# Performance work log

Hardware: AMD Instinct MI355X
Metric: run time of the kernel (lower is better)

Reference implementation:

```python
import jax, jax.numpy as jnp
import numpy as np

K = 8                      # batch_k
NONZERO_CUTOFF = 1.4       # nonzero_loss_cutoff
MARGIN = 1.0               # F.triplet_margin_loss default (module's margin arg is unused)
PD_EPS = 1e-6              # torch pairwise_distance eps


def setup_inputs() -> dict:
    key = jax.random.key(0)
    x = jax.random.normal(key, (4096, 128), dtype=jnp.float32)
    return {"x": x}


def _sample_indices(x, key):
    """Distance-weighted negative sampling; returns (a_idx, p_idx, n_idx), each [n*(K-1)]."""
    n, d = x.shape
    # per-row L2 normalize (eps added to norm, as in original)
    xn = x / (jnp.sqrt(jnp.sum(x * x, axis=1, keepdims=True)) + 1e-5)
    # pairwise euclidean distance; identity added under sqrt exactly as original
    sq = jnp.sum(xn * xn, axis=1, keepdims=True)               # [n,1]
    dist2 = sq + sq.T - 2.0 * (xn @ xn.T)                       # [n,n]
    dist = jnp.sqrt(dist2 + jnp.eye(n, dtype=x.dtype))          # [n,n]
    # distance-weighted sampling log-weights (Wu et al.)
    log_w = (2.0 - d) * jnp.log(dist) - (d - 3) / 2.0 * jnp.log(1.0 - 0.25 * dist * dist)
    w = jnp.exp(log_w - jnp.max(log_w))
    # block mask: same-block pairs excluded
    block = jnp.arange(n) // K                                  # [n]
    mask = (block[:, None] != block[None, :]).astype(x.dtype)
    w = w * mask * (dist < NONZERO_CUTOFF).astype(x.dtype)
    row_sum = jnp.sum(w, axis=1, keepdims=True)
    # rows where weights are degenerate fall back to uniform (original's try/except)
    valid = jnp.isfinite(row_sum) & (row_sum > 0) & jnp.all(jnp.isfinite(w), axis=1, keepdims=True)
    logits = jnp.where(valid, jnp.where(w > 0, jnp.log(w), -jnp.inf), 0.0)   # [n,n]
    # batched categorical sampling via Gumbel-max: K-1 negatives per anchor
    g = jax.random.gumbel(key, (n, K - 1, n), dtype=jnp.float32)
    n_idx = jnp.argmax(logits[:, None, :] + g, axis=-1).reshape(-1)          # [n*(K-1)]
    # anchor/positive pairs: for each i, all other members of its block
    r = jnp.arange(n) % K                                       # position in block
    off = jnp.arange(K - 1)
    p_off = jnp.where(off[None, :] < r[:, None], off[None, :], off[None, :] + 1)
    p_idx = (block[:, None] * K + p_off).reshape(-1)            # [n*(K-1)]
    a_idx = jnp.repeat(jnp.arange(n), K - 1)                    # [n*(K-1)]
    return a_idx, p_idx, n_idx


def reference(x) -> jnp.ndarray:
    key = jax.random.key(42)
    a_idx, p_idx, n_idx = _sample_indices(x, key)
    a, p, ng = x[a_idx], x[p_idx], x[n_idx]
    d_ap = jnp.sqrt(jnp.sum((a - p + PD_EPS) ** 2, axis=1))
    d_an = jnp.sqrt(jnp.sum((a - ng + PD_EPS) ** 2, axis=1))
    return jnp.mean(jnp.maximum(d_ap - d_an + MARGIN, 0.0))
```

## Files before the change

kernel.cpp:

```cpp
#include <hip/hip_runtime.h>
#include <stdint.h>

#define NROWS 4096
#define DIM   128
#define KB    8
#define NS    7
#define TCH   16
#define HALF_CNT 58720256u

typedef __bf16 v8bf __attribute__((ext_vector_type(8)));
typedef float  v4f  __attribute__((ext_vector_type(4)));

__device__ __forceinline__ uint32_t rotl32(uint32_t x, int r) {
    return (x << r) | (x >> (32 - r));
}

__device__ __forceinline__ void threefry2x32(uint32_t c0, uint32_t c1,
                                             uint32_t& o0, uint32_t& o1) {
    const uint32_t ks0 = 0u;
    const uint32_t ks1 = 42u;
    const uint32_t ks2 = 0x1BD11BDAu ^ ks0 ^ ks1;
    uint32_t x0 = c0 + ks0;
    uint32_t x1 = c1 + ks1;
#define TF_R(r) { x0 += x1; x1 = rotl32(x1, r); x1 ^= x0; }
    TF_R(13) TF_R(15) TF_R(26) TF_R(6)
    x0 += ks1; x1 += ks2 + 1u;
    TF_R(17) TF_R(29) TF_R(16) TF_R(24)
    x0 += ks2; x1 += ks0 + 2u;
    TF_R(13) TF_R(15) TF_R(26) TF_R(6)
    x0 += ks0; x1 += ks1 + 3u;
    TF_R(17) TF_R(29) TF_R(16) TF_R(24)
    x0 += ks1; x1 += ks2 + 4u;
    TF_R(13) TF_R(15) TF_R(26) TF_R(6)
    x0 += ks2; x1 += ks0 + 5u;
#undef TF_R
    o0 = x0; o1 = x1;
}

__device__ __forceinline__ float gumbel_of(uint32_t b) {
    float f = __uint_as_float((b >> 9) | 0x3f800000u) - 1.0f;
    float u = f + 1.17549435e-38f;
    float l1 = __log2f(u);
    float inner = -0.69314718055994531f * l1;
    float l2 = __log2f(inner);
    return -0.69314718055994531f * l2;
}

__global__ void knorm(const float* __restrict__ x, __bf16* __restrict__ xh,
                      __bf16* __restrict__ xl, float* __restrict__ sqv) {
    const int i = blockIdx.x;
    const int t = threadIdx.x;
    float2 v = ((const float2*)(x + (size_t)i * DIM))[t];
    float s = v.x * v.x + v.y * v.y;
#pragma unroll
    for (int m = 32; m > 0; m >>= 1) s += __shfl_xor(s, m, 64);
    float norm = sqrtf(s) + 1e-5f;
    float ox = v.x / norm, oy = v.y / norm;
    __bf16 hx = (__bf16)ox, hy = (__bf16)oy;
    float lx = ox - (float)hx, ly = oy - (float)hy;
    union { __bf16 b[2]; uint32_t u; } ph, pl;
    ph.b[0] = hx; ph.b[1] = hy;
    pl.b[0] = (__bf16)lx; pl.b[1] = (__bf16)ly;
    ((uint32_t*)xh)[i * 64 + t] = ph.u;
    ((uint32_t*)xl)[i * 64 + t] = pl.u;
    float s2 = ox * ox + oy * oy;
#pragma unroll
    for (int m = 32; m > 0; m >>= 1) s2 += __shfl_xor(s2, m, 64);
    if (t == 0) sqv[i] = s2;
}

__global__ __launch_bounds__(256, 2) void ksample(
        const __bf16* __restrict__ xh, const __bf16* __restrict__ xl,
        const float* __restrict__ sqv,
        float* __restrict__ pV, int* __restrict__ pI) {
    const int lane  = threadIdx.x & 63;
    const int chunk = (blockIdx.x << 2) + (threadIdx.x >> 6);
    const int grp   = blockIdx.y;
    const int rlo = lane & 15;
    const int khi = lane >> 4;

    const int afr = grp * 8 + (rlo >> 1) + ((rlo & 1) << 11);
    v8bf ah[4], al[4];
#pragma unroll
    for (int ks = 0; ks < 4; ++ks) {
        const size_t off = (size_t)afr * DIM + ks * 32 + khi * 8;
        ah[ks] = *(const v8bf*)(xh + off);
        al[ks] = *(const v8bf*)(xl + off);
    }

    const int base = grp * 8 + khi * 2;
    float sqA[4];
    sqA[0] = sqv[base];
    sqA[1] = sqv[base + 2048];
    sqA[2] = sqv[base + 1];
    sqA[3] = sqv[base + 2049];
    const uint32_t P0 = (uint32_t)base;
    const uint32_t P1 = (uint32_t)(base + 1);

    float    bestV[4][NS];
    uint32_t bestP[4];
#pragma unroll
    for (int q = 0; q < 4; ++q) {
        bestP[q] = 0u;
#pragma unroll
        for (int j = 0; j < NS; ++j) bestV[q][j] = -INFINITY;
    }

    const int tcol0 = chunk * 256 + rlo;

    v8bf bhn[4], bln[4];
    float sqn;
    {
        const size_t boff = (size_t)tcol0 * DIM + khi * 8;
#pragma unroll
        for (int ks = 0; ks < 4; ++ks) {
            bhn[ks] = *(const v8bf*)(xh + boff + ks * 32);
            bln[ks] = *(const v8bf*)(xl + boff + ks * 32);
        }
        sqn = sqv[tcol0];
    }

#pragma unroll 1
    for (int cg = 0; cg < 16; ++cg) {
        v8bf bhc[4], blc[4];
#pragma unroll
        for (int ks = 0; ks < 4; ++ks) { bhc[ks] = bhn[ks]; blc[ks] = bln[ks]; }
        const float sqB = sqn;
        const int tcol = tcol0 + cg * 16;

        if (cg < 15) {
            const size_t boff = (size_t)(tcol + 16) * DIM + khi * 8;
#pragma unroll
            for (int ks = 0; ks < 4; ++ks) {
                bhn[ks] = *(const v8bf*)(xh + boff + ks * 32);
                bln[ks] = *(const v8bf*)(xl + boff + ks * 32);
            }
            sqn = sqv[tcol + 16];
        }

        v4f acc1 = {0.f, 0.f, 0.f, 0.f};
        v4f acc2 = {0.f, 0.f, 0.f, 0.f};
        v4f acc3 = {0.f, 0.f, 0.f, 0.f};
#pragma unroll
        for (int ks = 0; ks < 4; ++ks) {
            acc1 = __builtin_amdgcn_mfma_f32_16x16x32_bf16(ah[ks], bhc[ks], acc1, 0, 0, 0);
            acc2 = __builtin_amdgcn_mfma_f32_16x16x32_bf16(ah[ks], blc[ks], acc2, 0, 0, 0);
            acc3 = __builtin_amdgcn_mfma_f32_16x16x32_bf16(al[ks], bhc[ks], acc3, 0, 0, 0);
        }

        const int tBlk = tcol >> 3;
        const bool bd0 = (tBlk != grp);
        const bool bd1 = (tBlk != grp + 256);

        float lg[4];
#pragma unroll
        for (int q = 0; q < 4; ++q) {
            float dot = acc1[q] + acc2[q] + acc3[q];
            float d2  = fmaf(-2.0f, dot, sqA[q] + sqB);
            float l1  = __log2f(d2);
            float t2  = fmaf(-0.25f, d2, 1.0f);
            float l2  = __log2f(t2);
            float lw  = fmaf(-43.66827237527655f, l1, -43.32169878499658f * l2);
            bool incl = (d2 < 1.96f) && ((q & 1) ? bd1 : bd0);
            lg[q] = incl ? lw : -INFINITY;
        }

        const uint32_t tB = (uint32_t)tcol;
#pragma unroll
        for (int j = 0; j < NS; ++j) {
            uint32_t L0 = ((P0 * 7u + (uint32_t)j) << 12) + tB;
            uint32_t L1 = ((P1 * 7u + (uint32_t)j) << 12) + tB;
            uint32_t o0, o1, o2, o3;
            threefry2x32(L0, L0 + HALF_CNT, o0, o1);
            threefry2x32(L1, L1 + HALF_CNT, o2, o3);
            float vv[4];
            vv[0] = lg[0] + gumbel_of(o0);
            vv[1] = lg[1] + gumbel_of(o1);
            vv[2] = lg[2] + gumbel_of(o2);
            vv[3] = lg[3] + gumbel_of(o3);
            const uint32_t keep = ~(0xFu << (4 * j));
            const uint32_t put  = ((uint32_t)cg) << (4 * j);
#pragma unroll
            for (int q = 0; q < 4; ++q) {
                bool gt = vv[q] > bestV[q][j];
                uint32_t np = (bestP[q] & keep) | put;
                bestV[q][j] = gt ? vv[q] : bestV[q][j];
                bestP[q]    = gt ? np : bestP[q];
            }
        }
    }

#pragma unroll
    for (int q = 0; q < 4; ++q) {
        const int a = base + (q >> 1) + ((q & 1) << 11);
#pragma unroll
        for (int j = 0; j < NS; ++j) {
            float v = bestV[q][j];
            int idx = tcol0 + (int)((bestP[q] >> (4 * j)) & 0xFu) * 16;
#pragma unroll
            for (int m = 1; m < 16; m <<= 1) {
                float v2 = __shfl_xor(v, m, 16);
                int   i2 = __shfl_xor(idx, m, 16);
                if (v2 > v || (v2 == v && i2 < idx)) { v = v2; idx = i2; }
            }
            if (rlo == 0) {
                size_t s = ((size_t)a * NS + j) * TCH + chunk;
                pV[s] = v;
                pI[s] = idx;
            }
        }
    }
}

__global__ void kcombine(const float* __restrict__ pV, const int* __restrict__ pI,
                         int* __restrict__ nidx) {
    int s = blockIdx.x * 256 + threadIdx.x;
    if (s >= NROWS * NS) return;
    float bv = -INFINITY;
    int bi = 0x7FFFFFFF;
#pragma unroll
    for (int c = 0; c < TCH; ++c) {
        float v = pV[(size_t)s * TCH + c];
        int idx = pI[(size_t)s * TCH + c];
        if (v > bv || (v == bv && idx < bi)) { bv = v; bi = idx; }
    }
    nidx[s] = (bv == -INFINITY) ? -1 : bi;
}

__global__ void kfixup(int* __restrict__ nidx) {
    const int i = blockIdx.x;
    if (nidx[(size_t)i * NS] >= 0) return;
    const int lane = threadIdx.x;
    for (int j = 0; j < NS; ++j) {
        float bv = -INFINITY;
        int bi = 0x7FFFFFFF;
        for (int t = lane; t < NROWS; t += 64) {
            uint32_t o0, o1;
            float g;
            if (i < 2048) {
                uint32_t L = (((uint32_t)(i * NS + j)) << 12) + (uint32_t)t;
                threefry2x32(L, L + HALF_CNT, o0, o1);
                g = gumbel_of(o0);
            } else {
                uint32_t L = (((uint32_t)((i - 2048) * NS + j)) << 12) + (uint32_t)t;
                threefry2x32(L, L + HALF_CNT, o0, o1);
                g = gumbel_of(o1);
            }
            if (g > bv) { bv = g; bi = t; }
        }
#pragma unroll
        for (int m = 1; m < 64; m <<= 1) {
            float v2 = __shfl_xor(bv, m, 64);
            int   i2 = __shfl_xor(bi, m, 64);
            if (v2 > bv || (v2 == bv && i2 < bi)) { bv = v2; bi = i2; }
        }
        if (lane == 0) nidx[i * NS + j] = bi;
    }
}

__global__ void kloss(const float* __restrict__ x, const int* __restrict__ nidx,
                      float* __restrict__ loss) {
    int s = blockIdx.x * 256 + threadIdx.x;
    if (s >= NROWS * NS) return;
    int i = s / NS, j = s - i * NS;
    int r = i & (KB - 1), blk = i >> 3;
    int po = (j < r) ? j : j + 1;
    int p = blk * KB + po;
    int n = nidx[s] & (NROWS - 1);
    const float4* A  = (const float4*)(x + (size_t)i * DIM);
    const float4* P  = (const float4*)(x + (size_t)p * DIM);
    const float4* Ng = (const float4*)(x + (size_t)n * DIM);
    float sap = 0.0f, san = 0.0f;
#pragma unroll 8
    for (int k = 0; k < DIM / 4; ++k) {
        float4 a = A[k], pv = P[k], nv = Ng[k];
        float d;
        d = a.x - pv.x + 1e-6f; sap += d * d;
        d = a.y - pv.y + 1e-6f; sap += d * d;
        d = a.z - pv.z + 1e-6f; sap += d * d;
        d = a.w - pv.w + 1e-6f; sap += d * d;
        d = a.x - nv.x + 1e-6f; san += d * d;
        d = a.y - nv.y + 1e-6f; san += d * d;
        d = a.z - nv.z + 1e-6f; san += d * d;
        d = a.w - nv.w + 1e-6f; san += d * d;
    }
    loss[s] = fmaxf(sqrtf(sap) - sqrtf(san) + 1.0f, 0.0f);
}

__global__ void kreduce(const float* __restrict__ loss, float* __restrict__ out) {
    __shared__ float part[4];
    const int tid = threadIdx.x;
    float sum = 0.0f;
    for (int s = tid; s < NROWS * NS; s += 256) sum += loss[s];
#pragma unroll
    for (int m = 32; m > 0; m >>= 1) sum += __shfl_xor(sum, m, 64);
    if ((tid & 63) == 0) part[tid >> 6] = sum;
    __syncthreads();
    if (tid == 0) out[0] = (part[0] + part[1] + part[2] + part[3]) / 28672.0f;
}

extern "C" void kernel_launch(void* const* d_in, const int* in_sizes, int n_in,
                              void* d_out, int out_size, void* d_ws, size_t ws_size,
                              hipStream_t stream) {
    const float* x = (const float*)d_in[0];
    float* out = (float*)d_out;

    __bf16* xh   = (__bf16*)d_ws;
    __bf16* xl   = xh + NROWS * DIM;
    float*  sqv  = (float*)(xl + NROWS * DIM);
    float*  pV   = sqv + NROWS;
    int*    pI   = (int*)(pV + NROWS * NS * TCH);
    int*    nidx = pI + NROWS * NS * TCH;
    float*  loss = (float*)(nidx + NROWS * NS);

    knorm<<<NROWS, 64, 0, stream>>>(x, xh, xl, sqv);
    ksample<<<dim3(TCH / 4, 256), 256, 0, stream>>>(xh, xl, sqv, pV, pI);
    kcombine<<<(NROWS * NS + 255) / 256, 256, 0, stream>>>(pV, pI, nidx);
    kfixup<<<NROWS, 64, 0, stream>>>(nidx);
    kloss<<<(NROWS * NS + 255) / 256, 256, 0, stream>>>(x, nidx, loss);
    kreduce<<<1, 256, 0, stream>>>(loss, out);
}
```

Measured before the change: 222.1 us.

## Compact eligible candidates before Gumbel sampling to skip masked entries

Splits the fused distance-and-sampling kernel into two passes. The first computes distance logits and stream-compacts the included columns (distance under cutoff, different block) per row pair into global buffers using ballot and atomic counters. The second generates threefry Gumbel noise only for the compacted candidates and reduces the argmax per sample. This avoids running the RNG on entries whose logit is minus infinity, but it adds roughly 80 MB of workspace traffic, atomics, and a memset. It falls back to the old path when the workspace is too small, and argmax ties now depend on the order of compacted entries.

```diff
diff --git a/kernel.cpp b/kernel.cpp
--- a/kernel.cpp
+++ b/kernel.cpp
@@ -6,6 +6,7 @@
 #define KB    8
 #define NS    7
 #define TCH   16
+#define NPAIR 2048
 #define HALF_CNT 58720256u
 
 typedef __bf16 v8bf __attribute__((ext_vector_type(8)));
@@ -69,6 +70,187 @@
     if (t == 0) sqv[i] = s2;
 }
 
+__global__ __launch_bounds__(256, 2) void kdist(
+        const __bf16* __restrict__ xh, const __bf16* __restrict__ xl,
+        const float* __restrict__ sqv,
+        int* __restrict__ cnt, unsigned short* __restrict__ t16,
+        float2* __restrict__ lgp) {
+    const int lane  = threadIdx.x & 63;
+    const int chunk = (blockIdx.x << 2) + (threadIdx.x >> 6);
+    const int grp   = blockIdx.y;
+    const int rlo = lane & 15;
+    const int khi = lane >> 4;
+
+    const int afr = grp * 8 + (rlo >> 1) + ((rlo & 1) << 11);
+    v8bf ah[4], al[4];
+#pragma unroll
+    for (int ks = 0; ks < 4; ++ks) {
+        const size_t off = (size_t)afr * DIM + ks * 32 + khi * 8;
+        ah[ks] = *(const v8bf*)(xh + off);
+        al[ks] = *(const v8bf*)(xl + off);
+    }
+
+    const int base = grp * 8 + khi * 2;
+    float sqA[4];
+    sqA[0] = sqv[base];
+    sqA[1] = sqv[base + 2048];
+    sqA[2] = sqv[base + 1];
+    sqA[3] = sqv[base + 2049];
+
+    const int tcol0 = chunk * 256 + rlo;
+
+    v8bf bhn[4], bln[4];
+    float sqn;
+    {
+        const size_t boff = (size_t)tcol0 * DIM + khi * 8;
+#pragma unroll
+        for (int ks = 0; ks < 4; ++ks) {
+            bhn[ks] = *(const v8bf*)(xh + boff + ks * 32);
+            bln[ks] = *(const v8bf*)(xl + boff + ks * 32);
+        }
+        sqn = sqv[tcol0];
+    }
+
+#pragma unroll 1
+    for (int cg = 0; cg < 16; ++cg) {
+        v8bf bhc[4], blc[4];
+#pragma unroll
+        for (int ks = 0; ks < 4; ++ks) { bhc[ks] = bhn[ks]; blc[ks] = bln[ks]; }
+        const float sqB = sqn;
+        const int tcol = tcol0 + cg * 16;
+
+        if (cg < 15) {
+            const size_t boff = (size_t)(tcol + 16) * DIM + khi * 8;
+#pragma unroll
+            for (int ks = 0; ks < 4; ++ks) {
+                bhn[ks] = *(const v8bf*)(xh + boff + ks * 32);
+                bln[ks] = *(const v8bf*)(xl + boff + ks * 32);
+            }
+            sqn = sqv[tcol + 16];
+        }
+
+        v4f acc1 = {0.f, 0.f, 0.f, 0.f};
+        v4f acc2 = {0.f, 0.f, 0.f, 0.f};
+        v4f acc3 = {0.f, 0.f, 0.f, 0.f};
+#pragma unroll
+        for (int ks = 0; ks < 4; ++ks) {
+            acc1 = __builtin_amdgcn_mfma_f32_16x16x32_bf16(ah[ks], bhc[ks], acc1, 0, 0, 0);
+            acc2 = __builtin_amdgcn_mfma_f32_16x16x32_bf16(ah[ks], blc[ks], acc2, 0, 0, 0);
+            acc3 = __builtin_amdgcn_mfma_f32_16x16x32_bf16(al[ks], bhc[ks], acc3, 0, 0, 0);
+        }
+
+        const int tBlk = tcol >> 3;
+        const bool bd0 = (tBlk != grp);
+        const bool bd1 = (tBlk != grp + 256);
+
+        float lg[4];
+        bool  ic[4];
+#pragma unroll
+        for (int q = 0; q < 4; ++q) {
+            float dot = acc1[q] + acc2[q] + acc3[q];
+            float d2  = fmaf(-2.0f, dot, sqA[q] + sqB);
+            float l1  = __log2f(d2);
+            float t2  = fmaf(-0.25f, d2, 1.0f);
+            float l2  = __log2f(t2);
+            float lw  = fmaf(-43.66827237527655f, l1, -43.32169878499658f * l2);
+            bool incl = (d2 < 1.96f) && ((q & 1) ? bd1 : bd0);
+            ic[q] = incl;
+            lg[q] = incl ? lw : -INFINITY;
+        }
+
+        const bool uA = ic[0] | ic[1];
+        const bool uB = ic[2] | ic[3];
+        unsigned long long ballA = __ballot(uA);
+        unsigned long long ballB = __ballot(uB);
+        unsigned int subA = (unsigned int)((ballA >> (khi * 16)) & 0xFFFFull);
+        unsigned int subB = (unsigned int)((ballB >> (khi * 16)) & 0xFFFFull);
+        int oldA = 0, oldB = 0;
+        if (rlo == 0) {
+            oldA = atomicAdd(&cnt[base], __popc(subA));
+            oldB = atomicAdd(&cnt[base + 1], __popc(subB));
+        }
+        oldA = __shfl(oldA, khi * 16, 64);
+        oldB = __shfl(oldB, khi * 16, 64);
+        const unsigned int below = (1u << rlo) - 1u;
+        if (uA) {
+            int slot = oldA + __popc(subA & below);
+            t16[(size_t)base * 4096 + slot] = (unsigned short)tcol;
+            lgp[(size_t)base * 4096 + slot] = make_float2(lg[0], lg[1]);
+        }
+        if (uB) {
+            int slot = oldB + __popc(subB & below);
+            t16[(size_t)(base + 1) * 4096 + slot] = (unsigned short)tcol;
+            lgp[(size_t)(base + 1) * 4096 + slot] = make_float2(lg[2], lg[3]);
+        }
+    }
+}
+
+__global__ __launch_bounds__(256, 2) void kgum(
+        const int* __restrict__ cnt, const unsigned short* __restrict__ t16,
+        const float2* __restrict__ lgp, int* __restrict__ nidx) {
+    const int p    = blockIdx.x;
+    const int tid  = threadIdx.x;
+    const int lane = tid & 63;
+    const int wid  = tid >> 6;
+    const int n    = cnt[p];
+    const size_t bp = (size_t)p * 4096;
+    const uint32_t pb = ((uint32_t)p * 7u) << 12;
+
+    float bv[2][NS];
+    int   bt[2][NS];
+#pragma unroll
+    for (int r = 0; r < 2; ++r)
+#pragma unroll
+        for (int j = 0; j < NS; ++j) { bv[r][j] = -INFINITY; bt[r][j] = 0x7FFFFFFF; }
+
+#pragma unroll 1
+    for (int e = tid; e < n; e += 256) {
+        const uint32_t t = t16[bp + e];
+        const float2 lg = lgp[bp + e];
+#pragma unroll
+        for (int j = 0; j < NS; ++j) {
+            uint32_t L = pb + ((uint32_t)j << 12) + t;
+            uint32_t o0, o1;
+            threefry2x32(L, L + HALF_CNT, o0, o1);
+            float v0 = lg.x + gumbel_of(o0);
+            float v1 = lg.y + gumbel_of(o1);
+            if (v0 > bv[0][j] || (v0 == bv[0][j] && (int)t < bt[0][j])) { bv[0][j] = v0; bt[0][j] = (int)t; }
+            if (v1 > bv[1][j] || (v1 == bv[1][j] && (int)t < bt[1][j])) { bv[1][j] = v1; bt[1][j] = (int)t; }
+        }
+    }
+
+    __shared__ float sV[4][2][NS];
+    __shared__ int   sT[4][2][NS];
+#pragma unroll
+    for (int r = 0; r < 2; ++r)
+#pragma unroll
+        for (int j = 0; j < NS; ++j) {
+            float v = bv[r][j];
+            int   t = bt[r][j];
+#pragma unroll
+            for (int m = 1; m < 64; m <<= 1) {
+                float v2 = __shfl_xor(v, m, 64);
+                int   t2 = __shfl_xor(t, m, 64);
+                if (v2 > v || (v2 == v && t2 < t)) { v = v2; t = t2; }
+            }
+            if (lane == 0) { sV[wid][r][j] = v; sT[wid][r][j] = t; }
+        }
+    __syncthreads();
+    if (tid < 2 * NS) {
+        const int r = tid / NS, j = tid - r * NS;
+        float v = sV[0][r][j];
+        int   t = sT[0][r][j];
+#pragma unroll
+        for (int w = 1; w < 4; ++w) {
+            float v2 = sV[w][r][j];
+            int   t2 = sT[w][r][j];
+            if (v2 > v || (v2 == v && t2 < t)) { v = v2; t = t2; }
+        }
+        const int row = p + r * 2048;
+        nidx[row * NS + j] = (v == -INFINITY) ? -1 : t;
+    }
+}
+
 __global__ __launch_bounds__(256, 2) void ksample(
         const __bf16* __restrict__ xh, const __bf16* __restrict__ xl,
         const float* __restrict__ sqv,
@@ -87,7 +269,6 @@
         ah[ks] = *(const v8bf*)(xh + off);
         al[ks] = *(const v8bf*)(xl + off);
     }
-
     const int base = grp * 8 + khi * 2;
     float sqA[4];
     sqA[0] = sqv[base];
@@ -105,7 +286,6 @@
 #pragma unroll
         for (int j = 0; j < NS; ++j) bestV[q][j] = -INFINITY;
     }
-
     const int tcol0 = chunk * 256 + rlo;
 
     v8bf bhn[4], bln[4];
@@ -127,7 +307,6 @@
         for (int ks = 0; ks < 4; ++ks) { bhc[ks] = bhn[ks]; blc[ks] = bln[ks]; }
         const float sqB = sqn;
         const int tcol = tcol0 + cg * 16;
-
         if (cg < 15) {
             const size_t boff = (size_t)(tcol + 16) * DIM + khi * 8;
 #pragma unroll
@@ -137,7 +316,6 @@
             }
             sqn = sqv[tcol + 16];
         }
-
         v4f acc1 = {0.f, 0.f, 0.f, 0.f};
         v4f acc2 = {0.f, 0.f, 0.f, 0.f};
         v4f acc3 = {0.f, 0.f, 0.f, 0.f};
@@ -147,11 +325,9 @@
             acc2 = __builtin_amdgcn_mfma_f32_16x16x32_bf16(ah[ks], blc[ks], acc2, 0, 0, 0);
             acc3 = __builtin_amdgcn_mfma_f32_16x16x32_bf16(al[ks], bhc[ks], acc3, 0, 0, 0);
         }
-
         const int tBlk = tcol >> 3;
         const bool bd0 = (tBlk != grp);
         const bool bd1 = (tBlk != grp + 256);
-
         float lg[4];
 #pragma unroll
         for (int q = 0; q < 4; ++q) {
@@ -164,7 +340,6 @@
             bool incl = (d2 < 1.96f) && ((q & 1) ? bd1 : bd0);
             lg[q] = incl ? lw : -INFINITY;
         }
-
         const uint32_t tB = (uint32_t)tcol;
 #pragma unroll
         for (int j = 0; j < NS; ++j) {
@@ -189,7 +364,6 @@
             }
         }
     }
-
 #pragma unroll
     for (int q = 0; q < 4; ++q) {
         const int a = base + (q >> 1) + ((q & 1) << 11);
@@ -305,17 +479,39 @@
     const float* x = (const float*)d_in[0];
     float* out = (float*)d_out;
 
-    __bf16* xh   = (__bf16*)d_ws;
-    __bf16* xl   = xh + NROWS * DIM;
-    float*  sqv  = (float*)(xl + NROWS * DIM);
-    float*  pV   = sqv + NROWS;
-    int*    pI   = (int*)(pV + NROWS * NS * TCH);
-    int*    nidx = pI + NROWS * NS * TCH;
-    float*  loss = (float*)(nidx + NROWS * NS);
+    uint8_t* w = (uint8_t*)d_ws;
+    size_t off = 0;
+    auto take = [&](size_t bytes) {
+        void* p = w + off;
+        off = (off + bytes + 255) & ~(size_t)255;
+        return p;
+    };
+    __bf16* xh   = (__bf16*)take((size_t)NROWS * DIM * 2);
+    __bf16* xl   = (__bf16*)take((size_t)NROWS * DIM * 2);
+    float*  sqv  = (float*)take((size_t)NROWS * 4);
+    int*    nidx = (int*)take((size_t)NROWS * NS * 4);
+    float*  loss = (float*)take((size_t)NROWS * NS * 4);
+    int*    cnt  = (int*)take((size_t)NPAIR * 4);
+    const size_t prefix = off;
+    const size_t t16_b = (size_t)NPAIR * 4096 * 2;
+    const size_t lgp_b = (size_t)NPAIR * 4096 * 8;
+    const size_t NEED_BIG = prefix + ((t16_b + 255) & ~(size_t)255) + lgp_b;
 
     knorm<<<NROWS, 64, 0, stream>>>(x, xh, xl, sqv);
-    ksample<<<dim3(TCH / 4, 256), 256, 0, stream>>>(xh, xl, sqv, pV, pI);
-    kcombine<<<(NROWS * NS + 255) / 256, 256, 0, stream>>>(pV, pI, nidx);
+
+    if (ws_size >= NEED_BIG) {
+        unsigned short* t16 = (unsigned short*)take(t16_b);
+        float2*         lgp = (float2*)take(lgp_b);
+        hipMemsetAsync(cnt, 0, NPAIR * sizeof(int), stream);
+        kdist<<<dim3(TCH / 4, 256), 256, 0, stream>>>(xh, xl, sqv, cnt, t16, lgp);
+        kgum<<<NPAIR, 256, 0, stream>>>(cnt, t16, lgp, nidx);
+    } else {
+        float* pV = (float*)take((size_t)NROWS * NS * TCH * 4);
+        int*   pI = (int*)take((size_t)NROWS * NS * TCH * 4);
+        ksample<<<dim3(TCH / 4, 256), 256, 0, stream>>>(xh, xl, sqv, pV, pI);
+        kcombine<<<(NROWS * NS + 255) / 256, 256, 0, stream>>>(pV, pI, nidx);
+    }
+
     kfixup<<<NROWS, 64, 0, stream>>>(nidx);
     kloss<<<(NROWS * NS + 255) / 256, 256, 0, stream>>>(x, nidx, loss);
     kreduce<<<1, 256, 0, stream>>>(loss, out);
```

Result: slower. 231.2 us (+4.1%).
